# Optimization experiments

Measured on AMD Instinct MI355X. Metric: run time of the kernel, lower is better.

## Reference

```python
import jax, jax.numpy as jnp
import numpy as np

N, G, S = 51200, 128, 400  # nodes, graphs, nodes-per-graph
E, IN, H, OUT = 819200, 128, 128, 10


def _graph_conv(x, src, dst, W_rel, b_rel, W_root):
    # PyG GraphConv (aggr='add'): lin_rel(sum_{j->i} x_j) + lin_root(x_i)
    agg = jax.ops.segment_sum(x[src], dst, num_segments=N)  # [N, d]
    return agg @ W_rel + b_rel + x @ W_root


def _mixup(x, lam, perm):
    return x * lam + (1.0 - lam) * x[perm]


def setup_inputs() -> dict:
    key = jax.random.key(0)
    ks = jax.random.split(key, 12)
    rng = np.random.default_rng(0)

    x0 = jax.random.normal(ks[0], (N, IN), dtype=jnp.float32)
    edge_index = jax.random.randint(ks[1], (2, E), 0, N, dtype=jnp.int64)
    lam = jax.random.uniform(ks[2], (1,), dtype=jnp.float32)
    ptr = jnp.arange(0, N + 1, S, dtype=jnp.int64)            # [G+1]
    batch = jnp.repeat(jnp.arange(G, dtype=jnp.int64), S)     # [N]

    def seg_perm():
        return jnp.asarray(np.concatenate(
            [g * S + rng.permutation(S) for g in range(G)]), dtype=jnp.int64)

    perm1, perm2, perm3 = seg_perm(), seg_perm(), seg_perm()

    def lin(k, fan_in, fan_out):
        bound = 1.0 / np.sqrt(fan_in)
        return jax.random.uniform(k, (fan_in, fan_out), jnp.float32, -bound, bound)

    params = {
        'W1_rel': lin(ks[3], IN, H), 'b1_rel': jnp.zeros((H,), jnp.float32),
        'W1_root': lin(ks[4], IN, H),
        'W2_rel': lin(ks[5], H, H), 'b2_rel': jnp.zeros((H,), jnp.float32),
        'W2_root': lin(ks[6], H, H),
        'W_lin': lin(ks[7], H, OUT), 'b_lin': jnp.zeros((OUT,), jnp.float32),
    }
    return dict(x0=x0, edge_index=edge_index, lam=lam, ptr=ptr, batch=batch,
                perm1=perm1, perm2=perm2, perm3=perm3, **params)


def reference(x0, edge_index, lam, ptr, batch, perm1, perm2, perm3,
              W1_rel, b1_rel, W1_root, W2_rel, b2_rel, W2_root, W_lin, b_lin):
    src, dst = edge_index[0], edge_index[1]
    l = lam[0]

    x1 = jax.nn.relu(_graph_conv(x0, src, dst, W1_rel, b1_rel, W1_root))
    x1 = _mixup(x1, l, perm1)  # dropout p=0.4 is identity in eval mode

    x2 = jax.nn.relu(_graph_conv(x1, src, dst, W2_rel, b2_rel, W2_root))
    x2 = _mixup(x2, l, perm2)

    # NOTE: original forward reuses conv2 for the third layer (conv3 unused)
    x3 = jax.nn.relu(_graph_conv(x2, src, dst, W2_rel, b2_rel, W2_root))
    x3 = _mixup(x3, l, perm3)

    pooled = jax.ops.segment_sum(x3, batch, num_segments=G)  # [G, H]
    logits = pooled @ W_lin + b_lin                          # [G, OUT]
    return jax.nn.log_softmax(logits, axis=-1)
```

## Files before the change

### kernel.cpp

```cpp
#include <hip/hip_runtime.h>

#define N_NODES 51200
#define N_EDGES 819200
#define HDIM 128
#define NGRAPH 128
#define SEG 400
#define NOUT 10
#define SLOT 64

#define HISTW (N_NODES / 4)
#define NBLK 200
#define EPB (N_EDGES / NBLK)
#define SEGS 8
#define BPSEG (NBLK / SEGS)

#define LDSW 264

typedef unsigned short ushort_t;
typedef unsigned int uint_t;
typedef __attribute__((ext_vector_type(8))) short bf16x8;
typedef __attribute__((ext_vector_type(16))) float f32x16;

static __device__ __forceinline__ unsigned short f2bf(float f) {
    unsigned int u = __float_as_uint(f);
    unsigned int r = (u + 0x7fffu + ((u >> 16) & 1u)) >> 16;
    return (unsigned short)r;
}
static __device__ __forceinline__ float bf2f(unsigned short h) {
    return __uint_as_float(((unsigned int)h) << 16);
}


__global__ void k_prep(const float* __restrict__ x, ushort_t* __restrict__ xbuf,
                       const float* __restrict__ W1rel, const float* __restrict__ W1root,
                       const float* __restrict__ W2rel, const float* __restrict__ W2root,
                       ushort_t* __restrict__ Wfrag1, ushort_t* __restrict__ Wfrag2,
                       float* __restrict__ pooled) {
    int b = blockIdx.x;
    if (b < 6400) {
        int idx = b * 256 + threadIdx.x;
        int row = idx >> 5;
        int c4 = (idx & 31) * 4;
        float4 v = *(const float4*)(x + (size_t)row * HDIM + c4);
        ushort4 h;
        h.x = f2bf(v.x); h.y = f2bf(v.y); h.z = f2bf(v.z); h.w = f2bf(v.w);
        *(ushort4*)(xbuf + (size_t)row * HDIM + c4) = h;
    } else if (b < 6656) {
        int w2 = (b >= 6528);
        int tid = (b - (w2 ? 6528 : 6400)) * 256 + threadIdx.x;
        const float* Wrel  = w2 ? W2rel : W1rel;
        const float* Wroot = w2 ? W2root : W1root;
        ushort_t* dstF     = w2 ? Wfrag2 : Wfrag1;
        int j = tid & 7;
        int l = (tid >> 3) & 63;
        int s = (tid >> 9) & 15;
        int t = tid >> 13;
        int k = 16 * s + (l >> 5) * 8 + j;
        int n = 32 * t + (l & 31);
        float v = (k < HDIM) ? Wrel[(size_t)k * HDIM + n]
                             : Wroot[(size_t)(k - HDIM) * HDIM + n];
        dstF[tid] = f2bf(v);
    } else {
        int i = (b - 6656) * 256 + threadIdx.x;
        pooled[i] = 0.f;
    }
}


__global__ __launch_bounds__(256) void k_count(const int* __restrict__ dst,
                                               uint_t* __restrict__ bh) {
    __shared__ uint_t hist[HISTW];
    int b = blockIdx.x, tid = threadIdx.x;
    for (int i = tid; i < HISTW; i += 256) hist[i] = 0u;
    __syncthreads();
    const int4* d4 = (const int4*)dst + b * (EPB / 4);
#pragma unroll
    for (int p = 0; p < 4; ++p) {
        int4 d = d4[p * 256 + tid];
        atomicAdd(&hist[((uint_t)d.x) >> 2], 1u << ((d.x & 3) * 8));
        atomicAdd(&hist[((uint_t)d.y) >> 2], 1u << ((d.y & 3) * 8));
        atomicAdd(&hist[((uint_t)d.z) >> 2], 1u << ((d.z & 3) * 8));
        atomicAdd(&hist[((uint_t)d.w) >> 2], 1u << ((d.w & 3) * 8));
    }
    __syncthreads();
    for (int i = tid; i < HISTW; i += 256) bh[(size_t)b * HISTW + i] = hist[i];
}


__global__ __launch_bounds__(256) void k_prefix(uint_t* __restrict__ bh,
                                                int* __restrict__ cnt) {
    __shared__ uint_t segsum[SEGS][32];
    int ci = threadIdx.x & 31;
    int seg = threadIdx.x >> 5;
    int c = blockIdx.x * 32 + ci;
    uint_t v[BPSEG];
    uint_t sum = 0;
#pragma unroll
    for (int k = 0; k < BPSEG; ++k) {
        v[k] = bh[(size_t)(seg * BPSEG + k) * HISTW + c];
        sum += v[k];
    }
    segsum[seg][ci] = sum;
    __syncthreads();
    uint_t run = 0;
    for (int s = 0; s < seg; ++s) run += segsum[s][ci];
#pragma unroll
    for (int k = 0; k < BPSEG; ++k) {
        bh[(size_t)(seg * BPSEG + k) * HISTW + c] = run;
        run += v[k];
    }
    if (seg == SEGS - 1) {
        int4 o;
        o.x = (int)(run & 0xffu);
        o.y = (int)((run >> 8) & 0xffu);
        o.z = (int)((run >> 16) & 0xffu);
        o.w = (int)((run >> 24) & 0xffu);
        *(int4*)(cnt + 4 * c) = o;
    }
}


__global__ __launch_bounds__(256) void k_place(const int* __restrict__ src,
                                               const int* __restrict__ dst,
                                               const uint_t* __restrict__ bh,
                                               ushort_t* __restrict__ col2) {
    __shared__ uint_t hist[HISTW];
    int b = blockIdx.x, tid = threadIdx.x;
    for (int i = tid; i < HISTW; i += 256) hist[i] = bh[(size_t)b * HISTW + i];
    __syncthreads();
    const int4* d4 = (const int4*)dst + b * (EPB / 4);
    const int4* s4 = (const int4*)src + b * (EPB / 4);
#pragma unroll
    for (int p = 0; p < 4; ++p) {
        int4 d = d4[p * 256 + tid];
        int4 s = s4[p * 256 + tid];
#define PLACE1(dd, ss)                                                        \
        do {                                                                  \
            uint_t w = (uint_t)(dd);                                          \
            int sh = (int)(w & 3u) * 8;                                       \
            uint_t old = atomicAdd(&hist[w >> 2], 1u << sh);                  \
            col2[(size_t)w * SLOT + ((old >> sh) & 0xffu)] = (ushort_t)(ss);  \
        } while (0)
        PLACE1(d.x, s.x);
        PLACE1(d.y, s.y);
        PLACE1(d.z, s.z);
        PLACE1(d.w, s.w);
#undef PLACE1
    }
}


template<int POOL>
__global__ __launch_bounds__(256) void k_layer(const ushort_t* __restrict__ xbuf,
                                               const int* __restrict__ cnt,
                                               const ushort_t* __restrict__ col,
                                               const ushort_t* __restrict__ Wfrag,
                                               const float* __restrict__ bias,
                                               ushort_t* __restrict__ y,
                                               float* __restrict__ pooled) {
    __shared__ ushort_t At[32][LDSW];
    int tid = threadIdx.x;
    int w = tid >> 6;
    int lane = tid & 63;
    int il = lane & 15;
    int qe = lane >> 4;
    int row0 = blockIdx.x * 32;

#pragma unroll
    for (int p = 0; p < 2; ++p) {
        int rl = w * 8 + p * 4 + qe;
        uint4 v = *(const uint4*)(xbuf + (size_t)(row0 + rl) * HDIM + il * 8);
        *(uint4*)&At[rl][HDIM + il * 8] = v;
    }

    const ushort_t* xsrc = xbuf + (size_t)il * 8;
    for (int i = 0; i < 8; ++i) {
        int rl = w * 8 + i;
        int node = row0 + rl;
        int beg = node * SLOT;
        int end = beg + cnt[node];

        float a[4][8];
#pragma unroll
        for (int j = 0; j < 4; ++j)
#pragma unroll
            for (int k = 0; k < 8; ++k) a[j][k] = 0.f;

        int e = beg;
        for (; e + 16 <= end; e += 16) {
            int c[4];
#pragma unroll
            for (int j = 0; j < 4; ++j) c[j] = (int)col[e + 4 * j + qe];
#pragma unroll
            for (int j = 0; j < 4; ++j) {
                uint4 v = *(const uint4*)(xsrc + (size_t)c[j] * HDIM);
                a[j][0] += __uint_as_float(v.x << 16);
                a[j][1] += __uint_as_float(v.x & 0xffff0000u);
                a[j][2] += __uint_as_float(v.y << 16);
                a[j][3] += __uint_as_float(v.y & 0xffff0000u);
                a[j][4] += __uint_as_float(v.z << 16);
                a[j][5] += __uint_as_float(v.z & 0xffff0000u);
                a[j][6] += __uint_as_float(v.w << 16);
                a[j][7] += __uint_as_float(v.w & 0xffff0000u);
            }
        }
        for (; e + 4 <= end; e += 4) {
            int c = (int)col[e + qe];
            uint4 v = *(const uint4*)(xsrc + (size_t)c * HDIM);
            a[0][0] += __uint_as_float(v.x << 16);
            a[0][1] += __uint_as_float(v.x & 0xffff0000u);
            a[0][2] += __uint_as_float(v.y << 16);
            a[0][3] += __uint_as_float(v.y & 0xffff0000u);
            a[0][4] += __uint_as_float(v.z << 16);
            a[0][5] += __uint_as_float(v.z & 0xffff0000u);
            a[0][6] += __uint_as_float(v.w << 16);
            a[0][7] += __uint_as_float(v.w & 0xffff0000u);
        }
        if (e < end) {
            int idx = e + qe;
            bool ok = idx < end;
            int c = (int)col[ok ? idx : e];
            uint4 v = *(const uint4*)(xsrc + (size_t)c * HDIM);
            a[1][0] += ok ? __uint_as_float(v.x << 16) : 0.f;
            a[1][1] += ok ? __uint_as_float(v.x & 0xffff0000u) : 0.f;
            a[1][2] += ok ? __uint_as_float(v.y << 16) : 0.f;
            a[1][3] += ok ? __uint_as_float(v.y & 0xffff0000u) : 0.f;
            a[1][4] += ok ? __uint_as_float(v.z << 16) : 0.f;
            a[1][5] += ok ? __uint_as_float(v.z & 0xffff0000u) : 0.f;
            a[1][6] += ok ? __uint_as_float(v.w << 16) : 0.f;
            a[1][7] += ok ? __uint_as_float(v.w & 0xffff0000u) : 0.f;
        }

        float s[8];
#pragma unroll
        for (int k = 0; k < 8; ++k) {
            s[k] = (a[0][k] + a[1][k]) + (a[2][k] + a[3][k]);
            s[k] += __shfl_xor(s[k], 16);
            s[k] += __shfl_xor(s[k], 32);
        }

        if (qe == 0) {
            uint4 o;
            o.x = (uint_t)f2bf(s[0]) | ((uint_t)f2bf(s[1]) << 16);
            o.y = (uint_t)f2bf(s[2]) | ((uint_t)f2bf(s[3]) << 16);
            o.z = (uint_t)f2bf(s[4]) | ((uint_t)f2bf(s[5]) << 16);
            o.w = (uint_t)f2bf(s[6]) | ((uint_t)f2bf(s[7]) << 16);
            *(uint4*)&At[rl][il * 8] = o;
        }
    }
    __syncthreads();

    int m = lane & 31;
    int half = lane >> 5;
    f32x16 acc = (f32x16)(0.f);
    float bb = bias[w * 32 + m];
    const ushort_t* arow = &At[m][half * 8];
    const ushort_t* wf = Wfrag + (size_t)lane * 8;

#pragma unroll
    for (int s = 0; s < 16; ++s) {
        bf16x8 afrag = *(const bf16x8*)(arow + s * 16);
        bf16x8 bfrag = *(const bf16x8*)(wf + (size_t)(w * 16 + s) * 512);
        acc = __builtin_amdgcn_mfma_f32_32x32x16_bf16(afrag, bfrag, acc, 0, 0, 0);
    }

    if (POOL == 0) {
        __syncthreads();
#pragma unroll
        for (int r = 0; r < 16; ++r) {
            int rowL = (r & 3) + 8 * (r >> 2) + 4 * half;
            At[rowL][w * 32 + m] = f2bf(fmaxf(acc[r] + bb, 0.f));
        }
        __syncthreads();
#pragma unroll
        for (int it = 0; it < 2; ++it) {
            int c = it * 256 + tid;
            int row = c >> 4;
            int sg = c & 15;
            *(int4*)(y + (size_t)(row0 + row) * HDIM + sg * 8) = *(const int4*)&At[row][sg * 8];
        }
    } else {
        int g0 = row0 / SEG;
        int bnd = (g0 + 1) * SEG;
        int straddle = (row0 + 31 >= bnd);
        float s0 = 0.f, s1 = 0.f;
#pragma unroll
        for (int r = 0; r < 16; ++r) {
            int row = row0 + (r & 3) + 8 * (r >> 2) + 4 * half;
            float v = fmaxf(acc[r] + bb, 0.f);
            if (row < bnd) s0 += v; else s1 += v;
        }
        s0 += __shfl_xor(s0, 32);
        s1 += __shfl_xor(s1, 32);
        if (half == 0) {
            int coln = w * 32 + m;
            atomicAdd(&pooled[g0 * HDIM + coln], s0);
            if (straddle) atomicAdd(&pooled[(g0 + 1) * HDIM + coln], s1);
        }
    }
}


__global__ void k_mixup_toA(const ushort_t* __restrict__ y, const int* __restrict__ perm,
                            const float* __restrict__ lam, ushort_t* __restrict__ xbuf) {
    int idx = blockIdx.x * 256 + threadIdx.x;
    int row = idx >> 5;
    int c4 = (idx & 31) * 4;
    float l = lam[0];
    float om = 1.f - l;
    int p = perm[row];
    ushort4 a = *(const ushort4*)(y + (size_t)row * HDIM + c4);
    ushort4 b = *(const ushort4*)(y + (size_t)p * HDIM + c4);
    ushort4 o;
    o.x = f2bf(l * bf2f(a.x) + om * bf2f(b.x));
    o.y = f2bf(l * bf2f(a.y) + om * bf2f(b.y));
    o.z = f2bf(l * bf2f(a.z) + om * bf2f(b.z));
    o.w = f2bf(l * bf2f(a.w) + om * bf2f(b.w));
    *(ushort4*)(xbuf + (size_t)row * HDIM + c4) = o;
}


__global__ __launch_bounds__(64) void k_final(const float* __restrict__ pooled,
                                              const float* __restrict__ Wlin,
                                              const float* __restrict__ blin,
                                              float* __restrict__ out) {
    int g = blockIdx.x;
    int lane = threadIdx.x;
    float2 v = *(const float2*)(pooled + (size_t)g * HDIM + lane * 2);
    float p[NOUT];
#pragma unroll
    for (int o = 0; o < NOUT; ++o)
        p[o] = v.x * Wlin[(size_t)(2 * lane) * NOUT + o] +
               v.y * Wlin[(size_t)(2 * lane + 1) * NOUT + o];
#pragma unroll
    for (int mask = 1; mask < 64; mask <<= 1)
#pragma unroll
        for (int o = 0; o < NOUT; ++o) p[o] += __shfl_xor(p[o], mask);
    if (lane == 0) {
        float lg[NOUT];
        float mx = -1e30f;
#pragma unroll
        for (int o = 0; o < NOUT; ++o) { lg[o] = p[o] + blin[o]; mx = fmaxf(mx, lg[o]); }
        float se = 0.f;
#pragma unroll
        for (int o = 0; o < NOUT; ++o) se += expf(lg[o] - mx);
        float lse = mx + logf(se);
#pragma unroll
        for (int o = 0; o < NOUT; ++o) out[g * NOUT + o] = lg[o] - lse;
    }
}


extern "C" void kernel_launch(void* const* d_in, const int* in_sizes, int n_in,
                              void* d_out, int out_size, void* d_ws, size_t ws_size,
                              hipStream_t stream) {
    const float* x0     = (const float*)d_in[0];
    const int*   edge   = (const int*)d_in[1];
    const int*   src    = edge;
    const int*   dst    = edge + N_EDGES;
    const float* lam    = (const float*)d_in[2];
    const int*   perm1  = (const int*)d_in[5];
    const int*   perm2  = (const int*)d_in[6];
    const float* W1_rel = (const float*)d_in[8];
    const float* b1_rel = (const float*)d_in[9];
    const float* W1_root= (const float*)d_in[10];
    const float* W2_rel = (const float*)d_in[11];
    const float* b2_rel = (const float*)d_in[12];
    const float* W2_root= (const float*)d_in[13];
    const float* W_lin  = (const float*)d_in[14];
    const float* b_lin  = (const float*)d_in[15];
    float* out = (float*)d_out;

    char* w = (char*)d_ws;
    size_t off = 0;
    auto alloc = [&](size_t bytes) -> void* {
        void* p = w + off;
        off = (off + bytes + 255) & ~(size_t)255;
        return p;
    };
    int* cnt       = (int*)alloc((size_t)N_NODES * 4);
    ushort_t* col2 = (ushort_t*)alloc((size_t)N_NODES * SLOT * 2);
    ushort_t* xbuf   = (ushort_t*)alloc((size_t)N_NODES * HDIM * 2);
    ushort_t* ybuf   = (ushort_t*)alloc((size_t)N_NODES * HDIM * 2);
    ushort_t* Wfrag1 = (ushort_t*)alloc(32768 * 2);
    ushort_t* Wfrag2 = (ushort_t*)alloc(32768 * 2);
    float* pooled    = (float*)alloc((size_t)NGRAPH * HDIM * 4);

    uint_t* bh = (uint_t*)ybuf;

    k_prep<<<6720, 256, 0, stream>>>(x0, xbuf, W1_rel, W1_root, W2_rel, W2_root,
                                     Wfrag1, Wfrag2, pooled);
    k_count<<<NBLK, 256, 0, stream>>>(dst, bh);
    k_prefix<<<HISTW / 32, 256, 0, stream>>>(bh, cnt);
    k_place<<<NBLK, 256, 0, stream>>>(src, dst, bh, col2);

    const int layGrid = N_NODES / 32;
    const int elGrid  = (N_NODES * HDIM / 4) / 256;

    k_layer<0><<<layGrid, 256, 0, stream>>>(xbuf, cnt, col2, Wfrag1, b1_rel, ybuf, pooled);
    k_mixup_toA<<<elGrid, 256, 0, stream>>>(ybuf, perm1, lam, xbuf);
    k_layer<0><<<layGrid, 256, 0, stream>>>(xbuf, cnt, col2, Wfrag2, b2_rel, ybuf, pooled);
    k_mixup_toA<<<elGrid, 256, 0, stream>>>(ybuf, perm2, lam, xbuf);
    k_layer<1><<<layGrid, 256, 0, stream>>>(xbuf, cnt, col2, Wfrag2, b2_rel, ybuf, pooled);

    k_final<<<NGRAPH, 64, 0, stream>>>(pooled, W_lin, b_lin, out);
}
```

Measured before the change: 298.8 us.

## Split fused aggregate+GEMM layer into separate gather and GEMM kernels via interleaved A buffer

The per-layer kernel that did neighbor gathering and then the MFMA GEMM is split into a standalone aggregation kernel, with one node per wave, and a GEMM kernel. The two communicate through a [N,256] bf16 buffer that holds the aggregated features next to the node's own features. The gather runs at finer granularity with more blocks, which should give better latency hiding, and the GEMM becomes a plain tiled load. The cost is an extra global round trip of the aggregated tensor and one more launch per layer. Separately, the edge-count histogram is folded into the prep kernel to remove one launch.

```diff
diff --git a/kernel.cpp b/kernel.cpp
--- a/kernel.cpp
+++ b/kernel.cpp
@@ -3,6 +3,7 @@
 #define N_NODES 51200
 #define N_EDGES 819200
 #define HDIM 128
+#define AK 256
 #define NGRAPH 128
 #define SEG 400
 #define NOUT 10
@@ -31,59 +32,56 @@
 }
 
 
-__global__ void k_prep(const float* __restrict__ x, ushort_t* __restrict__ xbuf,
+__global__ void k_prep(const float* __restrict__ x, ushort_t* __restrict__ Abuf,
                        const float* __restrict__ W1rel, const float* __restrict__ W1root,
                        const float* __restrict__ W2rel, const float* __restrict__ W2root,
                        ushort_t* __restrict__ Wfrag1, ushort_t* __restrict__ Wfrag2,
-                       float* __restrict__ pooled) {
+                       float* __restrict__ pooled, const int* __restrict__ dst,
+                       uint_t* __restrict__ bh) {
+    __shared__ uint_t hist[HISTW];
     int b = blockIdx.x;
-    if (b < 6400) {
-        int idx = b * 256 + threadIdx.x;
+    int tid = threadIdx.x;
+    if (b < NBLK) {
+        for (int i = tid; i < HISTW; i += 256) hist[i] = 0u;
+        __syncthreads();
+        const int4* d4 = (const int4*)dst + b * (EPB / 4);
+#pragma unroll
+        for (int p = 0; p < 4; ++p) {
+            int4 d = d4[p * 256 + tid];
+            atomicAdd(&hist[((uint_t)d.x) >> 2], 1u << ((d.x & 3) * 8));
+            atomicAdd(&hist[((uint_t)d.y) >> 2], 1u << ((d.y & 3) * 8));
+            atomicAdd(&hist[((uint_t)d.z) >> 2], 1u << ((d.z & 3) * 8));
+            atomicAdd(&hist[((uint_t)d.w) >> 2], 1u << ((d.w & 3) * 8));
+        }
+        __syncthreads();
+        for (int i = tid; i < HISTW; i += 256) bh[(size_t)b * HISTW + i] = hist[i];
+    } else if (b < 6600) {
+        int idx = (b - NBLK) * 256 + tid;
         int row = idx >> 5;
         int c4 = (idx & 31) * 4;
         float4 v = *(const float4*)(x + (size_t)row * HDIM + c4);
         ushort4 h;
         h.x = f2bf(v.x); h.y = f2bf(v.y); h.z = f2bf(v.z); h.w = f2bf(v.w);
-        *(ushort4*)(xbuf + (size_t)row * HDIM + c4) = h;
-    } else if (b < 6656) {
-        int w2 = (b >= 6528);
-        int tid = (b - (w2 ? 6528 : 6400)) * 256 + threadIdx.x;
+        *(ushort4*)(Abuf + (size_t)row * AK + HDIM + c4) = h;
+    } else if (b < 6856) {
+        int w2 = (b >= 6728);
+        int t0 = (b - (w2 ? 6728 : 6600)) * 256 + tid;
         const float* Wrel  = w2 ? W2rel : W1rel;
         const float* Wroot = w2 ? W2root : W1root;
         ushort_t* dstF     = w2 ? Wfrag2 : Wfrag1;
-        int j = tid & 7;
-        int l = (tid >> 3) & 63;
-        int s = (tid >> 9) & 15;
-        int t = tid >> 13;
+        int j = t0 & 7;
+        int l = (t0 >> 3) & 63;
+        int s = (t0 >> 9) & 15;
+        int t = t0 >> 13;
         int k = 16 * s + (l >> 5) * 8 + j;
         int n = 32 * t + (l & 31);
         float v = (k < HDIM) ? Wrel[(size_t)k * HDIM + n]
                              : Wroot[(size_t)(k - HDIM) * HDIM + n];
-        dstF[tid] = f2bf(v);
+        dstF[t0] = f2bf(v);
     } else {
-        int i = (b - 6656) * 256 + threadIdx.x;
+        int i = (b - 6856) * 256 + tid;
         pooled[i] = 0.f;
     }
-}
-
-
-__global__ __launch_bounds__(256) void k_count(const int* __restrict__ dst,
-                                               uint_t* __restrict__ bh) {
-    __shared__ uint_t hist[HISTW];
-    int b = blockIdx.x, tid = threadIdx.x;
-    for (int i = tid; i < HISTW; i += 256) hist[i] = 0u;
-    __syncthreads();
-    const int4* d4 = (const int4*)dst + b * (EPB / 4);
-#pragma unroll
-    for (int p = 0; p < 4; ++p) {
-        int4 d = d4[p * 256 + tid];
-        atomicAdd(&hist[((uint_t)d.x) >> 2], 1u << ((d.x & 3) * 8));
-        atomicAdd(&hist[((uint_t)d.y) >> 2], 1u << ((d.y & 3) * 8));
-        atomicAdd(&hist[((uint_t)d.z) >> 2], 1u << ((d.z & 3) * 8));
-        atomicAdd(&hist[((uint_t)d.w) >> 2], 1u << ((d.w & 3) * 8));
-    }
-    __syncthreads();
-    for (int i = tid; i < HISTW; i += 256) bh[(size_t)b * HISTW + i] = hist[i];
 }
 
 
@@ -150,103 +148,107 @@
 }
 
 
+__global__ __launch_bounds__(256) void k_aggregate(ushort_t* __restrict__ Abuf,
+                                                   const int* __restrict__ cnt,
+                                                   const ushort_t* __restrict__ col) {
+    int wave = threadIdx.x >> 6;
+    int lane = threadIdx.x & 63;
+    int il = lane & 15;
+    int qe = lane >> 4;
+    int node = blockIdx.x * 4 + wave;
+    int beg = node * SLOT;
+    int end = beg + cnt[node];
+
+    const ushort_t* xsrc = Abuf + HDIM + (size_t)il * 8;
+
+    float a[4][8];
+#pragma unroll
+    for (int j = 0; j < 4; ++j)
+#pragma unroll
+        for (int k = 0; k < 8; ++k) a[j][k] = 0.f;
+
+    int e = beg;
+    for (; e + 16 <= end; e += 16) {
+        int c[4];
+#pragma unroll
+        for (int j = 0; j < 4; ++j) c[j] = (int)col[e + 4 * j + qe];
+#pragma unroll
+        for (int j = 0; j < 4; ++j) {
+            uint4 v = *(const uint4*)(xsrc + (size_t)c[j] * AK);
+            a[j][0] += __uint_as_float(v.x << 16);
+            a[j][1] += __uint_as_float(v.x & 0xffff0000u);
+            a[j][2] += __uint_as_float(v.y << 16);
+            a[j][3] += __uint_as_float(v.y & 0xffff0000u);
+            a[j][4] += __uint_as_float(v.z << 16);
+            a[j][5] += __uint_as_float(v.z & 0xffff0000u);
+            a[j][6] += __uint_as_float(v.w << 16);
+            a[j][7] += __uint_as_float(v.w & 0xffff0000u);
+        }
+    }
+    for (; e + 4 <= end; e += 4) {
+        int c = (int)col[e + qe];
+        uint4 v = *(const uint4*)(xsrc + (size_t)c * AK);
+        a[0][0] += __uint_as_float(v.x << 16);
+        a[0][1] += __uint_as_float(v.x & 0xffff0000u);
+        a[0][2] += __uint_as_float(v.y << 16);
+        a[0][3] += __uint_as_float(v.y & 0xffff0000u);
+        a[0][4] += __uint_as_float(v.z << 16);
+        a[0][5] += __uint_as_float(v.z & 0xffff0000u);
+        a[0][6] += __uint_as_float(v.w << 16);
+        a[0][7] += __uint_as_float(v.w & 0xffff0000u);
+    }
+    if (e < end) {
+        int idx = e + qe;
+        bool ok = idx < end;
+        int c = (int)col[ok ? idx : e];
+        uint4 v = *(const uint4*)(xsrc + (size_t)c * AK);
+        a[1][0] += ok ? __uint_as_float(v.x << 16) : 0.f;
+        a[1][1] += ok ? __uint_as_float(v.x & 0xffff0000u) : 0.f;
+        a[1][2] += ok ? __uint_as_float(v.y << 16) : 0.f;
+        a[1][3] += ok ? __uint_as_float(v.y & 0xffff0000u) : 0.f;
+        a[1][4] += ok ? __uint_as_float(v.z << 16) : 0.f;
+        a[1][5] += ok ? __uint_as_float(v.z & 0xffff0000u) : 0.f;
+        a[1][6] += ok ? __uint_as_float(v.w << 16) : 0.f;
+        a[1][7] += ok ? __uint_as_float(v.w & 0xffff0000u) : 0.f;
+    }
+
+    float s[8];
+#pragma unroll
+    for (int k = 0; k < 8; ++k) {
+        s[k] = (a[0][k] + a[1][k]) + (a[2][k] + a[3][k]);
+        s[k] += __shfl_xor(s[k], 16);
+        s[k] += __shfl_xor(s[k], 32);
+    }
+
+    if (qe == 0) {
+        uint4 o;
+        o.x = (uint_t)f2bf(s[0]) | ((uint_t)f2bf(s[1]) << 16);
+        o.y = (uint_t)f2bf(s[2]) | ((uint_t)f2bf(s[3]) << 16);
+        o.z = (uint_t)f2bf(s[4]) | ((uint_t)f2bf(s[5]) << 16);
+        o.w = (uint_t)f2bf(s[6]) | ((uint_t)f2bf(s[7]) << 16);
+        *(uint4*)(Abuf + (size_t)node * AK + il * 8) = o;
+    }
+}
+
+
 template<int POOL>
-__global__ __launch_bounds__(256) void k_layer(const ushort_t* __restrict__ xbuf,
-                                               const int* __restrict__ cnt,
-                                               const ushort_t* __restrict__ col,
-                                               const ushort_t* __restrict__ Wfrag,
-                                               const float* __restrict__ bias,
-                                               ushort_t* __restrict__ y,
-                                               float* __restrict__ pooled) {
+__global__ __launch_bounds__(256) void k_gemm256(const ushort_t* __restrict__ Abuf,
+                                                 const ushort_t* __restrict__ Wfrag,
+                                                 const float* __restrict__ bias,
+                                                 ushort_t* __restrict__ y,
+                                                 float* __restrict__ pooled) {
     __shared__ ushort_t At[32][LDSW];
     int tid = threadIdx.x;
     int w = tid >> 6;
     int lane = tid & 63;
-    int il = lane & 15;
-    int qe = lane >> 4;
     int row0 = blockIdx.x * 32;
 
 #pragma unroll
-    for (int p = 0; p < 2; ++p) {
-        int rl = w * 8 + p * 4 + qe;
-        uint4 v = *(const uint4*)(xbuf + (size_t)(row0 + rl) * HDIM + il * 8);
-        *(uint4*)&At[rl][HDIM + il * 8] = v;
-    }
-
-    const ushort_t* xsrc = xbuf + (size_t)il * 8;
-    for (int i = 0; i < 8; ++i) {
-        int rl = w * 8 + i;
-        int node = row0 + rl;
-        int beg = node * SLOT;
-        int end = beg + cnt[node];
-
-        float a[4][8];
-#pragma unroll
-        for (int j = 0; j < 4; ++j)
-#pragma unroll
-            for (int k = 0; k < 8; ++k) a[j][k] = 0.f;
-
-        int e = beg;
-        for (; e + 16 <= end; e += 16) {
-            int c[4];
-#pragma unroll
-            for (int j = 0; j < 4; ++j) c[j] = (int)col[e + 4 * j + qe];
-#pragma unroll
-            for (int j = 0; j < 4; ++j) {
-                uint4 v = *(const uint4*)(xsrc + (size_t)c[j] * HDIM);
-                a[j][0] += __uint_as_float(v.x << 16);
-                a[j][1] += __uint_as_float(v.x & 0xffff0000u);
-                a[j][2] += __uint_as_float(v.y << 16);
-                a[j][3] += __uint_as_float(v.y & 0xffff0000u);
-                a[j][4] += __uint_as_float(v.z << 16);
-                a[j][5] += __uint_as_float(v.z & 0xffff0000u);
-                a[j][6] += __uint_as_float(v.w << 16);
-                a[j][7] += __uint_as_float(v.w & 0xffff0000u);
-            }
-        }
-        for (; e + 4 <= end; e += 4) {
-            int c = (int)col[e + qe];
-            uint4 v = *(const uint4*)(xsrc + (size_t)c * HDIM);
-            a[0][0] += __uint_as_float(v.x << 16);
-            a[0][1] += __uint_as_float(v.x & 0xffff0000u);
-            a[0][2] += __uint_as_float(v.y << 16);
-            a[0][3] += __uint_as_float(v.y & 0xffff0000u);
-            a[0][4] += __uint_as_float(v.z << 16);
-            a[0][5] += __uint_as_float(v.z & 0xffff0000u);
-            a[0][6] += __uint_as_float(v.w << 16);
-            a[0][7] += __uint_as_float(v.w & 0xffff0000u);
-        }
-        if (e < end) {
-            int idx = e + qe;
-            bool ok = idx < end;
-            int c = (int)col[ok ? idx : e];
-            uint4 v = *(const uint4*)(xsrc + (size_t)c * HDIM);
-            a[1][0] += ok ? __uint_as_float(v.x << 16) : 0.f;
-            a[1][1] += ok ? __uint_as_float(v.x & 0xffff0000u) : 0.f;
-            a[1][2] += ok ? __uint_as_float(v.y << 16) : 0.f;
-            a[1][3] += ok ? __uint_as_float(v.y & 0xffff0000u) : 0.f;
-            a[1][4] += ok ? __uint_as_float(v.z << 16) : 0.f;
-            a[1][5] += ok ? __uint_as_float(v.z & 0xffff0000u) : 0.f;
-            a[1][6] += ok ? __uint_as_float(v.w << 16) : 0.f;
-            a[1][7] += ok ? __uint_as_float(v.w & 0xffff0000u) : 0.f;
-        }
-
-        float s[8];
-#pragma unroll
-        for (int k = 0; k < 8; ++k) {
-            s[k] = (a[0][k] + a[1][k]) + (a[2][k] + a[3][k]);
-            s[k] += __shfl_xor(s[k], 16);
-            s[k] += __shfl_xor(s[k], 32);
-        }
-
-        if (qe == 0) {
-            uint4 o;
-            o.x = (uint_t)f2bf(s[0]) | ((uint_t)f2bf(s[1]) << 16);
-            o.y = (uint_t)f2bf(s[2]) | ((uint_t)f2bf(s[3]) << 16);
-            o.z = (uint_t)f2bf(s[4]) | ((uint_t)f2bf(s[5]) << 16);
-            o.w = (uint_t)f2bf(s[6]) | ((uint_t)f2bf(s[7]) << 16);
-            *(uint4*)&At[rl][il * 8] = o;
-        }
+    for (int it = 0; it < 4; ++it) {
+        int idx = it * 256 + tid;
+        int r = idx >> 5;
+        int c16 = idx & 31;
+        *(uint4*)&At[r][c16 * 8] = *(const uint4*)(Abuf + (size_t)(row0 + r) * AK + c16 * 8);
     }
     __syncthreads();
 
@@ -302,7 +304,7 @@
 
 
 __global__ void k_mixup_toA(const ushort_t* __restrict__ y, const int* __restrict__ perm,
-                            const float* __restrict__ lam, ushort_t* __restrict__ xbuf) {
+                            const float* __restrict__ lam, ushort_t* __restrict__ Abuf) {
     int idx = blockIdx.x * 256 + threadIdx.x;
     int row = idx >> 5;
     int c4 = (idx & 31) * 4;
@@ -316,7 +318,7 @@
     o.y = f2bf(l * bf2f(a.y) + om * bf2f(b.y));
     o.z = f2bf(l * bf2f(a.z) + om * bf2f(b.z));
     o.w = f2bf(l * bf2f(a.w) + om * bf2f(b.w));
-    *(ushort4*)(xbuf + (size_t)row * HDIM + c4) = o;
+    *(ushort4*)(Abuf + (size_t)row * AK + HDIM + c4) = o;
 }
 
 
@@ -380,7 +382,7 @@
     };
     int* cnt       = (int*)alloc((size_t)N_NODES * 4);
     ushort_t* col2 = (ushort_t*)alloc((size_t)N_NODES * SLOT * 2);
-    ushort_t* xbuf   = (ushort_t*)alloc((size_t)N_NODES * HDIM * 2);
+    ushort_t* Abuf   = (ushort_t*)alloc((size_t)N_NODES * AK * 2);
     ushort_t* ybuf   = (ushort_t*)alloc((size_t)N_NODES * HDIM * 2);
     ushort_t* Wfrag1 = (ushort_t*)alloc(32768 * 2);
     ushort_t* Wfrag2 = (ushort_t*)alloc(32768 * 2);
@@ -388,20 +390,23 @@
 
     uint_t* bh = (uint_t*)ybuf;
 
-    k_prep<<<6720, 256, 0, stream>>>(x0, xbuf, W1_rel, W1_root, W2_rel, W2_root,
-                                     Wfrag1, Wfrag2, pooled);
-    k_count<<<NBLK, 256, 0, stream>>>(dst, bh);
+    k_prep<<<6920, 256, 0, stream>>>(x0, Abuf, W1_rel, W1_root, W2_rel, W2_root,
+                                     Wfrag1, Wfrag2, pooled, dst, bh);
     k_prefix<<<HISTW / 32, 256, 0, stream>>>(bh, cnt);
     k_place<<<NBLK, 256, 0, stream>>>(src, dst, bh, col2);
 
-    const int layGrid = N_NODES / 32;
-    const int elGrid  = (N_NODES * HDIM / 4) / 256;
-
-    k_layer<0><<<layGrid, 256, 0, stream>>>(xbuf, cnt, col2, Wfrag1, b1_rel, ybuf, pooled);
-    k_mixup_toA<<<elGrid, 256, 0, stream>>>(ybuf, perm1, lam, xbuf);
-    k_layer<0><<<layGrid, 256, 0, stream>>>(xbuf, cnt, col2, Wfrag2, b2_rel, ybuf, pooled);
-    k_mixup_toA<<<elGrid, 256, 0, stream>>>(ybuf, perm2, lam, xbuf);
-    k_layer<1><<<layGrid, 256, 0, stream>>>(xbuf, cnt, col2, Wfrag2, b2_rel, ybuf, pooled);
+    const int aggGrid  = N_NODES / 4;
+    const int gemmGrid = N_NODES / 32;
+    const int elGrid   = (N_NODES * HDIM / 4) / 256;
+
+    k_aggregate<<<aggGrid, 256, 0, stream>>>(Abuf, cnt, col2);
+    k_gemm256<0><<<gemmGrid, 256, 0, stream>>>(Abuf, Wfrag1, b1_rel, ybuf, pooled);
+    k_mixup_toA<<<elGrid, 256, 0, stream>>>(ybuf, perm1, lam, Abuf);
+    k_aggregate<<<aggGrid, 256, 0, stream>>>(Abuf, cnt, col2);
+    k_gemm256<0><<<gemmGrid, 256, 0, stream>>>(Abuf, Wfrag2, b2_rel, ybuf, pooled);
+    k_mixup_toA<<<elGrid, 256, 0, stream>>>(ybuf, perm2, lam, Abuf);
+    k_aggregate<<<aggGrid, 256, 0, stream>>>(Abuf, cnt, col2);
+    k_gemm256<1><<<gemmGrid, 256, 0, stream>>>(Abuf, Wfrag2, b2_rel, ybuf, pooled);
 
     k_final<<<NGRAPH, 64, 0, stream>>>(pooled, W_lin, b_lin, out);
 }
```

Result: faster. 264.3 us (-11.6%).
